# Kernel tuning notes

Hardware: AMD Instinct MI355X
Metric: run time of the kernel (lower is better)

The kernel has to match this reference:

```python
import jax, jax.numpy as jnp
import numpy as np

L, N, S, C = 128, 8, 16384, 256   # queries, batch, pixels (128x128), d_model
B, V = 256, 256                   # bottleneck channels, value depth
EPS_NORM = 1e-12                  # F.normalize eps
EPS_LN = 1e-5                     # LayerNorm eps


def _xavier(key, fan_out, fan_in):
    lim = np.sqrt(6.0 / (fan_in + fan_out)).astype(np.float32)
    return jax.random.uniform(key, (fan_out, fan_in), jnp.float32, -lim, lim)


def setup_inputs() -> dict:
    key = jax.random.key(0)
    ks = jax.random.split(key, 8)
    return {
        "tgt": jax.random.normal(ks[0], (L, N, C), jnp.float32),
        "memory": jax.random.normal(ks[1], (S, N, C), jnp.float32),
        "pos": jax.random.normal(ks[2], (S, N, C), jnp.float32),
        "query_pos": jax.random.normal(ks[3], (L, N, C), jnp.float32),
        "Wq": _xavier(ks[4], B, C), "bq": jnp.zeros((B,), jnp.float32),
        "Wp": _xavier(ks[5], B, C), "bp": jnp.zeros((B,), jnp.float32),
        "Wv": _xavier(ks[6], V, B), "bv": jnp.zeros((V,), jnp.float32),
        "Wo": _xavier(ks[7], C, V), "bo": jnp.zeros((C,), jnp.float32),
        "gamma": jnp.ones((C,), jnp.float32),
        "beta": jnp.zeros((C,), jnp.float32),
    }


def reference(tgt, memory, pos, query_pos, Wq, bq, Wp, bp, Wv, bv, Wo, bo, gamma, beta):
    q = tgt + query_pos                       # (L,N,C)
    k = memory + pos                          # (S,N,C)
    q_proj = q @ Wq.T + bq                    # (L,N,B)
    k_proj = k @ Wp.T + bp                    # (S,N,B)
    v_proj = k_proj @ Wv.T + bv               # (S,N,V)
    # F.normalize(k_proj, p=2, dim=-1)
    k_norm = k_proj / jnp.maximum(
        jnp.linalg.norm(k_proj, axis=-1, keepdims=True), EPS_NORM)
    mask_logits = jnp.einsum('lnc,snc->nls', q_proj, k_norm)  # (N,L,S)
    # hard top-1 assignment (detached in torch); one-hot einsum == direct gather
    idx = jnp.argmax(mask_logits, axis=-1)    # (N,L) int
    v_t = jnp.transpose(v_proj, (1, 0, 2))    # (N,S,V)
    kmeans = jnp.take_along_axis(v_t, idx[:, :, None], axis=1)  # (N,L,V)
    kmeans = jnp.transpose(kmeans, (1, 0, 2))  # (L,N,V)
    upd = kmeans @ Wo.T + bo                  # (L,N,C)
    x = tgt + upd                             # dropout p=0 -> identity
    mu = jnp.mean(x, axis=-1, keepdims=True)
    var = jnp.var(x, axis=-1, keepdims=True)
    return (x - mu) / jnp.sqrt(var + EPS_LN) * gamma + beta
```

## Files before the change

kernel.cpp:

```cpp
#include <hip/hip_runtime.h>
#include <stdint.h>

#define L_Q 128
#define N_B 8
#define S_P 16384

typedef _Float16 half8 __attribute__((ext_vector_type(8)));
typedef float f32x4 __attribute__((ext_vector_type(4)));


__global__ __launch_bounds__(256) void k_prep(
    const float* __restrict__ Wp, const float* __restrict__ Wv,
    const float* __restrict__ Wo,
    float* __restrict__ WpT, float* __restrict__ WvT, float* __restrict__ WoT,
    _Float16* __restrict__ Wp_hi, _Float16* __restrict__ Wp_lo,
    unsigned long long* __restrict__ packed) {
  int idx = (blockIdx.x << 8) + threadIdx.x;
  int r = idx >> 8, c = idx & 255;
  int t = (c << 8) + r;
  float wp = Wp[idx];
  WpT[t] = wp;
  WvT[t] = Wv[idx];
  WoT[t] = Wo[idx];
  _Float16 h = (_Float16)wp;
  Wp_hi[idx] = h;
  Wp_lo[idx] = (_Float16)(wp - (float)h);
  if (idx < N_B * L_Q) packed[idx] = 0ull;
}

__global__ __launch_bounds__(256) void k_qproj(
    const float* __restrict__ tgt, const float* __restrict__ qpos,
    const float* __restrict__ Wq, const float* __restrict__ bq,
    _Float16* __restrict__ q_hi, _Float16* __restrict__ q_lo) {
  __shared__ __align__(16) float q_lds[4][256];
  int tid = threadIdx.x;
  int r0 = blockIdx.x << 2;
  #pragma unroll
  for (int j = 0; j < 4; ++j) {
    int p = (j << 8) + tid;
    int rl = p >> 8, c = p & 255;
    int g = ((r0 + rl) << 8) + c;
    q_lds[rl][c] = tgt[g] + qpos[g];
  }
  __syncthreads();
  float bqv = bq[tid];
  float a0 = bqv, a1 = bqv, a2 = bqv, a3 = bqv;
  #pragma unroll 4
  for (int c = 0; c < 256; c += 4) {
    float4 w = *(const float4*)(Wq + (tid << 8) + c);
    a0 = fmaf(w.x, q_lds[0][c], fmaf(w.y, q_lds[0][c+1],
         fmaf(w.z, q_lds[0][c+2], fmaf(w.w, q_lds[0][c+3], a0))));
    a1 = fmaf(w.x, q_lds[1][c], fmaf(w.y, q_lds[1][c+1],
         fmaf(w.z, q_lds[1][c+2], fmaf(w.w, q_lds[1][c+3], a1))));
    a2 = fmaf(w.x, q_lds[2][c], fmaf(w.y, q_lds[2][c+1],
         fmaf(w.z, q_lds[2][c+2], fmaf(w.w, q_lds[2][c+3], a2))));
    a3 = fmaf(w.x, q_lds[3][c], fmaf(w.y, q_lds[3][c+1],
         fmaf(w.z, q_lds[3][c+2], fmaf(w.w, q_lds[3][c+3], a3))));
  }
  float av[4] = {a0, a1, a2, a3};
  #pragma unroll
  for (int rl = 0; rl < 4; ++rl) {
    int r = r0 + rl;
    int l = r >> 3, nn = r & 7;
    int o = (((nn << 7) + l) << 8) + tid;
    _Float16 h = (_Float16)av[rl];
    q_hi[o] = h;
    q_lo[o] = (_Float16)(av[rl] - (float)h);
  }
}

__global__ __launch_bounds__(256, 2) void k_main(
    const float* __restrict__ memory, const float* __restrict__ pos,
    const _Float16* __restrict__ Wp_hi, const _Float16* __restrict__ Wp_lo,
    const float* __restrict__ bp,
    const _Float16* __restrict__ q_hi, const _Float16* __restrict__ q_lo,
    unsigned long long* __restrict__ packed) {
  __shared__ __align__(16) unsigned short smu[2 * 64 * 256];
  unsigned short* a_hi = smu;
  unsigned short* a_lo = smu + 16384;

  int tid = threadIdx.x;
  int w = tid >> 6;
  int lane = tid & 63;
  int l15 = lane & 15, quad = lane >> 4;
  int n = blockIdx.y;
  int s_base = blockIdx.x << 6;

  {
    int half = tid >> 5;
    int chunk = tid & 31;
    int c0 = chunk << 3;
    #pragma unroll
    for (int it = 0; it < 8; ++it) {
      int srow = (it << 3) + half;
      int g = (((s_base + srow) << 3) + n) * 256 + c0;
      float4 m0 = *(const float4*)(memory + g);
      float4 m1 = *(const float4*)(memory + g + 4);
      float4 p0 = *(const float4*)(pos + g);
      float4 p1 = *(const float4*)(pos + g + 4);
      float f[8] = {m0.x + p0.x, m0.y + p0.y, m0.z + p0.z, m0.w + p0.w,
                    m1.x + p1.x, m1.y + p1.y, m1.z + p1.z, m1.w + p1.w};
      half8 hv, lv;
      #pragma unroll
      for (int j = 0; j < 8; ++j) {
        _Float16 h = (_Float16)f[j];
        hv[j] = h;
        lv[j] = (_Float16)(f[j] - (float)h);
      }
      int p = chunk ^ (srow & 15);
      *(half8*)(a_hi + (srow << 8) + (p << 3)) = hv;
      *(half8*)(a_lo + (srow << 8) + (p << 3)) = lv;
    }
  }
  __syncthreads();

  f32x4 acc1[4][4];
  #pragma unroll
  for (int m = 0; m < 4; ++m)
    #pragma unroll
    for (int bn = 0; bn < 4; ++bn) acc1[m][bn] = (f32x4)(0.0f);

  for (int kk = 0; kk < 8; ++kk) {
    int cofs = (kk << 5) + (quad << 3);
    half8 ah[4], al[4];
    #pragma unroll
    for (int m = 0; m < 4; ++m) {
      int s = (m << 4) + l15;
      int p = (cofs >> 3) ^ l15;
      ah[m] = *(const half8*)(a_hi + (s << 8) + (p << 3));
      al[m] = *(const half8*)(a_lo + (s << 8) + (p << 3));
    }
    #pragma unroll
    for (int bn = 0; bn < 4; ++bn) {
      int b = (w << 6) + (bn << 4) + l15;
      half8 wh = *(const half8*)(Wp_hi + (b << 8) + cofs);
      half8 wl = *(const half8*)(Wp_lo + (b << 8) + cofs);
      #pragma unroll
      for (int m = 0; m < 4; ++m) {
        acc1[m][bn] = __builtin_amdgcn_mfma_f32_16x16x32_f16(ah[m], wh, acc1[m][bn], 0, 0, 0);
        acc1[m][bn] = __builtin_amdgcn_mfma_f32_16x16x32_f16(ah[m], wl, acc1[m][bn], 0, 0, 0);
        acc1[m][bn] = __builtin_amdgcn_mfma_f32_16x16x32_f16(al[m], wh, acc1[m][bn], 0, 0, 0);
      }
    }
  }

  float bpv[4];
  #pragma unroll
  for (int bn = 0; bn < 4; ++bn) bpv[bn] = bp[(w << 6) + (bn << 4) + l15];
  float n2[4][4];
  #pragma unroll
  for (int m = 0; m < 4; ++m)
    #pragma unroll
    for (int r = 0; r < 4; ++r) {
      float s = 0.f;
      #pragma unroll
      for (int bn = 0; bn < 4; ++bn) {
        float v = acc1[m][bn][r] + bpv[bn];
        acc1[m][bn][r] = v;
        s = fmaf(v, v, s);
      }
      n2[m][r] = s;
    }
  #pragma unroll
  for (int off = 1; off < 16; off <<= 1)
    #pragma unroll
    for (int m = 0; m < 4; ++m)
      #pragma unroll
      for (int r = 0; r < 4; ++r) n2[m][r] += __shfl_xor(n2[m][r], off, 64);

  __syncthreads();
  if (l15 == 0) {
    #pragma unroll
    for (int m = 0; m < 4; ++m)
      #pragma unroll
      for (int r = 0; r < 4; ++r) {
        int i = (w << 6) + (m << 4) + (quad << 2) + r;
        unsigned u = __float_as_uint(n2[m][r]);
        smu[i << 1] = (unsigned short)u;
        smu[(i << 1) + 1] = (unsigned short)(u >> 16);
      }
  }
  __syncthreads();
  float rn[4][4];
  #pragma unroll
  for (int m = 0; m < 4; ++m)
    #pragma unroll
    for (int r = 0; r < 4; ++r) {
      int s = (m << 4) + (quad << 2) + r;
      float t = 0.f;
      #pragma unroll
      for (int ww = 0; ww < 4; ++ww) {
        int i = (ww << 6) + s;
        unsigned u = (unsigned)smu[i << 1] | ((unsigned)smu[(i << 1) + 1] << 16);
        t += __uint_as_float(u);
      }
      rn[m][r] = 1.f / fmaxf(sqrtf(t), 1e-12f);
    }
  __syncthreads();

  unsigned short* kn_hi = smu;
  unsigned short* kn_lo = smu + 16384;
  #pragma unroll
  for (int m = 0; m < 4; ++m)
    #pragma unroll
    for (int bn = 0; bn < 4; ++bn)
      #pragma unroll
      for (int r = 0; r < 4; ++r) {
        int s = (m << 4) + (quad << 2) + r;
        int b = (w << 6) + (bn << 4) + l15;
        float v = acc1[m][bn][r] * rn[m][r];
        _Float16 h = (_Float16)v;
        _Float16 lo = (_Float16)(v - (float)h);
        int p = (b >> 3) ^ (s & 15);
        int off = (s << 8) + (p << 3) + (b & 7);
        *(_Float16*)(kn_hi + off) = h;
        *(_Float16*)(kn_lo + off) = lo;
      }
  __syncthreads();

  f32x4 acc2[2][4];
  #pragma unroll
  for (int m = 0; m < 2; ++m)
    #pragma unroll
    for (int sn = 0; sn < 4; ++sn) acc2[m][sn] = (f32x4)(0.0f);

  const _Float16* qhb = q_hi + (n << 15);
  const _Float16* qlb = q_lo + (n << 15);
  for (int kk = 0; kk < 8; ++kk) {
    int b0 = (kk << 5) + (quad << 3);
    half8 qh[2], ql[2];
    #pragma unroll
    for (int m = 0; m < 2; ++m) {
      int l = (w << 5) + (m << 4) + l15;
      qh[m] = *(const half8*)(qhb + (l << 8) + b0);
      ql[m] = *(const half8*)(qlb + (l << 8) + b0);
    }
    #pragma unroll
    for (int sn = 0; sn < 4; ++sn) {
      int s = (sn << 4) + l15;
      int p = (b0 >> 3) ^ l15;
      half8 kh = *(const half8*)(kn_hi + (s << 8) + (p << 3));
      half8 kl = *(const half8*)(kn_lo + (s << 8) + (p << 3));
      #pragma unroll
      for (int m = 0; m < 2; ++m) {
        acc2[m][sn] = __builtin_amdgcn_mfma_f32_16x16x32_f16(qh[m], kh, acc2[m][sn], 0, 0, 0);
        acc2[m][sn] = __builtin_amdgcn_mfma_f32_16x16x32_f16(qh[m], kl, acc2[m][sn], 0, 0, 0);
        acc2[m][sn] = __builtin_amdgcn_mfma_f32_16x16x32_f16(ql[m], kh, acc2[m][sn], 0, 0, 0);
      }
    }
  }

  float mv[8];
  int mi[8];
  #pragma unroll
  for (int m = 0; m < 2; ++m)
    #pragma unroll
    for (int r = 0; r < 4; ++r) {
      int i = (m << 2) + r;
      mv[i] = acc2[m][0][r];
      mi[i] = s_base + l15;
      #pragma unroll
      for (int sn = 1; sn < 4; ++sn) {
        float v = acc2[m][sn][r];
        int si = s_base + (sn << 4) + l15;
        if (v > mv[i]) { mv[i] = v; mi[i] = si; }
      }
    }
  #pragma unroll
  for (int off = 1; off < 16; off <<= 1)
    #pragma unroll
    for (int i = 0; i < 8; ++i) {
      float ov = __shfl_xor(mv[i], off, 64);
      int oi = __shfl_xor(mi[i], off, 64);
      if (ov > mv[i] || (ov == mv[i] && oi < mi[i])) { mv[i] = ov; mi[i] = oi; }
    }
  if (l15 == 0) {
    #pragma unroll
    for (int i = 0; i < 8; ++i) {
      int m = i >> 2, r = i & 3;
      int l = (w << 5) + (m << 4) + (quad << 2) + r;
      unsigned ub = __float_as_uint(mv[i]);
      ub = (ub & 0x80000000u) ? ~ub : (ub | 0x80000000u);
      unsigned long long pk = ((unsigned long long)ub << 32) |
                              (unsigned long long)(16383u - (unsigned)mi[i]);
      atomicMax(packed + (n << 7) + l, pk);
    }
  }
}

__global__ __launch_bounds__(256) void k_final(
    const float* __restrict__ tgt,
    const float* __restrict__ memory, const float* __restrict__ pos,
    const float* __restrict__ WpT, const float* __restrict__ bp,
    const float* __restrict__ WvT, const float* __restrict__ bv,
    const float* __restrict__ WoT, const float* __restrict__ bo,
    const float* __restrict__ gamma, const float* __restrict__ beta,
    const unsigned long long* __restrict__ packed, float* __restrict__ out) {
  __shared__ __align__(16) float buf0[4][256];
  __shared__ __align__(16) float buf1[4][256];
  __shared__ __align__(16) float buf2[4][256];
  __shared__ float red[4][4][2];
  int tid = threadIdx.x;
  int r0 = blockIdx.x << 2;

  #pragma unroll
  for (int j = 0; j < 4; ++j) {
    int p = (j << 8) + tid;
    int rl = p >> 8, c = p & 255;
    int r = r0 + rl;
    int l = r >> 3, nn = r & 7;
    unsigned long long pk = packed[(nn << 7) + l];
    int sstar = (16383 - (int)(unsigned int)(pk & 0xffffffffu)) & 16383;
    int g = ((sstar << 3) + nn) * 256 + c;
    buf0[rl][c] = memory[g] + pos[g];
  }
  __syncthreads();

  float a[4];
  { float b0v = bp[tid];
    #pragma unroll
    for (int rl = 0; rl < 4; ++rl) a[rl] = b0v; }
  #pragma unroll 4
  for (int c = 0; c < 256; ++c) {
    float w = WpT[(c << 8) + tid];
    #pragma unroll
    for (int rl = 0; rl < 4; ++rl) a[rl] = fmaf(w, buf0[rl][c], a[rl]);
  }
  #pragma unroll
  for (int rl = 0; rl < 4; ++rl) buf1[rl][tid] = a[rl];
  __syncthreads();

  { float b0v = bv[tid];
    #pragma unroll
    for (int rl = 0; rl < 4; ++rl) a[rl] = b0v; }
  #pragma unroll 4
  for (int c = 0; c < 256; ++c) {
    float w = WvT[(c << 8) + tid];
    #pragma unroll
    for (int rl = 0; rl < 4; ++rl) a[rl] = fmaf(w, buf1[rl][c], a[rl]);
  }
  #pragma unroll
  for (int rl = 0; rl < 4; ++rl) buf2[rl][tid] = a[rl];
  __syncthreads();

  { float b0v = bo[tid];
    #pragma unroll
    for (int rl = 0; rl < 4; ++rl) a[rl] = b0v; }
  #pragma unroll 4
  for (int c = 0; c < 256; ++c) {
    float w = WoT[(c << 8) + tid];
    #pragma unroll
    for (int rl = 0; rl < 4; ++rl) a[rl] = fmaf(w, buf2[rl][c], a[rl]);
  }
  float x[4];
  #pragma unroll
  for (int rl = 0; rl < 4; ++rl)
    x[rl] = tgt[((r0 + rl) << 8) + tid] + a[rl];

  float s1[4], s2[4];
  #pragma unroll
  for (int rl = 0; rl < 4; ++rl) { s1[rl] = x[rl]; s2[rl] = x[rl] * x[rl]; }
  #pragma unroll
  for (int off = 1; off < 64; off <<= 1)
    #pragma unroll
    for (int rl = 0; rl < 4; ++rl) {
      s1[rl] += __shfl_xor(s1[rl], off, 64);
      s2[rl] += __shfl_xor(s2[rl], off, 64);
    }
  int wv = tid >> 6, ln = tid & 63;
  if (ln == 0) {
    #pragma unroll
    for (int rl = 0; rl < 4; ++rl) { red[wv][rl][0] = s1[rl]; red[wv][rl][1] = s2[rl]; }
  }
  __syncthreads();
  float g = gamma[tid], be = beta[tid];
  #pragma unroll
  for (int rl = 0; rl < 4; ++rl) {
    float S1 = red[0][rl][0] + red[1][rl][0] + red[2][rl][0] + red[3][rl][0];
    float S2 = red[0][rl][1] + red[1][rl][1] + red[2][rl][1] + red[3][rl][1];
    float mu = S1 * (1.f / 256.f);
    float var = S2 * (1.f / 256.f) - mu * mu;
    float rs = rsqrtf(var + 1e-5f);
    out[((r0 + rl) << 8) + tid] = (x[rl] - mu) * rs * g + be;
  }
}

extern "C" void kernel_launch(void* const* d_in, const int* in_sizes, int n_in,
                              void* d_out, int out_size, void* d_ws, size_t ws_size,
                              hipStream_t stream) {
  const float* tgt    = (const float*)d_in[0];
  const float* memory = (const float*)d_in[1];
  const float* pos    = (const float*)d_in[2];
  const float* qpos   = (const float*)d_in[3];
  const float* Wq     = (const float*)d_in[4];
  const float* bq     = (const float*)d_in[5];
  const float* Wp     = (const float*)d_in[6];
  const float* bp     = (const float*)d_in[7];
  const float* Wv     = (const float*)d_in[8];
  const float* bv     = (const float*)d_in[9];
  const float* Wo     = (const float*)d_in[10];
  const float* bo     = (const float*)d_in[11];
  const float* gamma  = (const float*)d_in[12];
  const float* beta   = (const float*)d_in[13];

  float* ws = (float*)d_ws;
  float* WpT = ws;
  float* WvT = ws + 65536;
  float* WoT = ws + 131072;
  _Float16* Wp_hi = (_Float16*)(ws + 196608);
  _Float16* Wp_lo = (_Float16*)(ws + 229376);
  _Float16* q_hi  = (_Float16*)(ws + 262144);
  _Float16* q_lo  = (_Float16*)(ws + 393216);
  unsigned long long* packed = (unsigned long long*)(ws + 524288);
  float* out = (float*)d_out;

  k_prep<<<256, 256, 0, stream>>>(Wp, Wv, Wo, WpT, WvT, WoT, Wp_hi, Wp_lo, packed);
  k_qproj<<<256, 256, 0, stream>>>(tgt, qpos, Wq, bq, q_hi, q_lo);
  dim3 gb(S_P / 64, N_B);
  k_main<<<gb, 256, 0, stream>>>(memory, pos, Wp_hi, Wp_lo, bp, q_hi, q_lo, packed);
  k_final<<<256, 256, 0, stream>>>(tgt, memory, pos, WpT, bp, WvT, bv,
                                   WoT, bo, gamma, beta, packed, out);
}
```

Measured before the change: 503.2 us.

## Halve k_main pixel tile for occupancy, merge prep and qproj kernels

Each k_main block now handles 32 pixels instead of 64. This halves LDS use and accumulator registers and raises the occupancy hint to 4 blocks per CU. The norm reduction uses a dedicated small shared array, which removes two block barriers. The weight-prep and query-projection kernels are fused into one launch to save a launch. In exchange, each block reloads the Wp and q fragments for half as many pixels, doubling global/L2 traffic for those operands, and there are twice as many atomic argmax updates.

```diff
diff --git a/kernel.cpp b/kernel.cpp
--- a/kernel.cpp
+++ b/kernel.cpp
@@ -9,32 +9,32 @@
 typedef float f32x4 __attribute__((ext_vector_type(4)));
 
 
-__global__ __launch_bounds__(256) void k_prep(
+__global__ __launch_bounds__(256) void k_prep_qproj(
     const float* __restrict__ Wp, const float* __restrict__ Wv,
     const float* __restrict__ Wo,
     float* __restrict__ WpT, float* __restrict__ WvT, float* __restrict__ WoT,
     _Float16* __restrict__ Wp_hi, _Float16* __restrict__ Wp_lo,
-    unsigned long long* __restrict__ packed) {
-  int idx = (blockIdx.x << 8) + threadIdx.x;
-  int r = idx >> 8, c = idx & 255;
-  int t = (c << 8) + r;
-  float wp = Wp[idx];
-  WpT[t] = wp;
-  WvT[t] = Wv[idx];
-  WoT[t] = Wo[idx];
-  _Float16 h = (_Float16)wp;
-  Wp_hi[idx] = h;
-  Wp_lo[idx] = (_Float16)(wp - (float)h);
-  if (idx < N_B * L_Q) packed[idx] = 0ull;
-}
-
-__global__ __launch_bounds__(256) void k_qproj(
+    unsigned long long* __restrict__ packed,
     const float* __restrict__ tgt, const float* __restrict__ qpos,
     const float* __restrict__ Wq, const float* __restrict__ bq,
     _Float16* __restrict__ q_hi, _Float16* __restrict__ q_lo) {
   __shared__ __align__(16) float q_lds[4][256];
   int tid = threadIdx.x;
-  int r0 = blockIdx.x << 2;
+  if (blockIdx.x < 256) {
+    int idx = (blockIdx.x << 8) + tid;
+    int r = idx >> 8, c = idx & 255;
+    int t = (c << 8) + r;
+    float wp = Wp[idx];
+    WpT[t] = wp;
+    WvT[t] = Wv[idx];
+    WoT[t] = Wo[idx];
+    _Float16 h = (_Float16)wp;
+    Wp_hi[idx] = h;
+    Wp_lo[idx] = (_Float16)(wp - (float)h);
+    if (idx < N_B * L_Q) packed[idx] = 0ull;
+    return;
+  }
+  int r0 = (blockIdx.x - 256) << 2;
   #pragma unroll
   for (int j = 0; j < 4; ++j) {
     int p = (j << 8) + tid;
@@ -69,29 +69,30 @@
   }
 }
 
-__global__ __launch_bounds__(256, 2) void k_main(
+__global__ __launch_bounds__(256, 4) void k_main(
     const float* __restrict__ memory, const float* __restrict__ pos,
     const _Float16* __restrict__ Wp_hi, const _Float16* __restrict__ Wp_lo,
     const float* __restrict__ bp,
     const _Float16* __restrict__ q_hi, const _Float16* __restrict__ q_lo,
     unsigned long long* __restrict__ packed) {
-  __shared__ __align__(16) unsigned short smu[2 * 64 * 256];
+  __shared__ __align__(16) unsigned short smu[2 * 32 * 256];
+  __shared__ float snorm[4][32];
   unsigned short* a_hi = smu;
-  unsigned short* a_lo = smu + 16384;
+  unsigned short* a_lo = smu + 8192;
 
   int tid = threadIdx.x;
   int w = tid >> 6;
   int lane = tid & 63;
   int l15 = lane & 15, quad = lane >> 4;
   int n = blockIdx.y;
-  int s_base = blockIdx.x << 6;
+  int s_base = blockIdx.x << 5;
 
   {
     int half = tid >> 5;
     int chunk = tid & 31;
     int c0 = chunk << 3;
     #pragma unroll
-    for (int it = 0; it < 8; ++it) {
+    for (int it = 0; it < 4; ++it) {
       int srow = (it << 3) + half;
       int g = (((s_base + srow) << 3) + n) * 256 + c0;
       float4 m0 = *(const float4*)(memory + g);
@@ -114,17 +115,17 @@
   }
   __syncthreads();
 
-  f32x4 acc1[4][4];
-  #pragma unroll
-  for (int m = 0; m < 4; ++m)
+  f32x4 acc1[2][4];
+  #pragma unroll
+  for (int m = 0; m < 2; ++m)
     #pragma unroll
     for (int bn = 0; bn < 4; ++bn) acc1[m][bn] = (f32x4)(0.0f);
 
   for (int kk = 0; kk < 8; ++kk) {
     int cofs = (kk << 5) + (quad << 3);
-    half8 ah[4], al[4];
-    #pragma unroll
-    for (int m = 0; m < 4; ++m) {
+    half8 ah[2], al[2];
+    #pragma unroll
+    for (int m = 0; m < 2; ++m) {
       int s = (m << 4) + l15;
       int p = (cofs >> 3) ^ l15;
       ah[m] = *(const half8*)(a_hi + (s << 8) + (p << 3));
@@ -136,7 +137,7 @@
       half8 wh = *(const half8*)(Wp_hi + (b << 8) + cofs);
       half8 wl = *(const half8*)(Wp_lo + (b << 8) + cofs);
       #pragma unroll
-      for (int m = 0; m < 4; ++m) {
+      for (int m = 0; m < 2; ++m) {
         acc1[m][bn] = __builtin_amdgcn_mfma_f32_16x16x32_f16(ah[m], wh, acc1[m][bn], 0, 0, 0);
         acc1[m][bn] = __builtin_amdgcn_mfma_f32_16x16x32_f16(ah[m], wl, acc1[m][bn], 0, 0, 0);
         acc1[m][bn] = __builtin_amdgcn_mfma_f32_16x16x32_f16(al[m], wh, acc1[m][bn], 0, 0, 0);
@@ -147,9 +148,9 @@
   float bpv[4];
   #pragma unroll
   for (int bn = 0; bn < 4; ++bn) bpv[bn] = bp[(w << 6) + (bn << 4) + l15];
-  float n2[4][4];
-  #pragma unroll
-  for (int m = 0; m < 4; ++m)
+  float n2[2][4];
+  #pragma unroll
+  for (int m = 0; m < 2; ++m)
     #pragma unroll
     for (int r = 0; r < 4; ++r) {
       float s = 0.f;
@@ -164,44 +165,32 @@
   #pragma unroll
   for (int off = 1; off < 16; off <<= 1)
     #pragma unroll
-    for (int m = 0; m < 4; ++m)
+    for (int m = 0; m < 2; ++m)
       #pragma unroll
       for (int r = 0; r < 4; ++r) n2[m][r] += __shfl_xor(n2[m][r], off, 64);
 
-  __syncthreads();
   if (l15 == 0) {
     #pragma unroll
-    for (int m = 0; m < 4; ++m)
-      #pragma unroll
-      for (int r = 0; r < 4; ++r) {
-        int i = (w << 6) + (m << 4) + (quad << 2) + r;
-        unsigned u = __float_as_uint(n2[m][r]);
-        smu[i << 1] = (unsigned short)u;
-        smu[(i << 1) + 1] = (unsigned short)(u >> 16);
-      }
-  }
-  __syncthreads();
-  float rn[4][4];
-  #pragma unroll
-  for (int m = 0; m < 4; ++m)
+    for (int m = 0; m < 2; ++m)
+      #pragma unroll
+      for (int r = 0; r < 4; ++r)
+        snorm[w][(m << 4) + (quad << 2) + r] = n2[m][r];
+  }
+  __syncthreads();
+  float rn[2][4];
+  #pragma unroll
+  for (int m = 0; m < 2; ++m)
     #pragma unroll
     for (int r = 0; r < 4; ++r) {
       int s = (m << 4) + (quad << 2) + r;
-      float t = 0.f;
-      #pragma unroll
-      for (int ww = 0; ww < 4; ++ww) {
-        int i = (ww << 6) + s;
-        unsigned u = (unsigned)smu[i << 1] | ((unsigned)smu[(i << 1) + 1] << 16);
-        t += __uint_as_float(u);
-      }
+      float t = snorm[0][s] + snorm[1][s] + snorm[2][s] + snorm[3][s];
       rn[m][r] = 1.f / fmaxf(sqrtf(t), 1e-12f);
     }
-  __syncthreads();
 
   unsigned short* kn_hi = smu;
-  unsigned short* kn_lo = smu + 16384;
-  #pragma unroll
-  for (int m = 0; m < 4; ++m)
+  unsigned short* kn_lo = smu + 8192;
+  #pragma unroll
+  for (int m = 0; m < 2; ++m)
     #pragma unroll
     for (int bn = 0; bn < 4; ++bn)
       #pragma unroll
@@ -218,11 +207,11 @@
       }
   __syncthreads();
 
-  f32x4 acc2[2][4];
-  #pragma unroll
-  for (int m = 0; m < 2; ++m)
-    #pragma unroll
-    for (int sn = 0; sn < 4; ++sn) acc2[m][sn] = (f32x4)(0.0f);
+  f32x4 acc2[2][2];
+  #pragma unroll
+  for (int m = 0; m < 2; ++m)
+    #pragma unroll
+    for (int sn = 0; sn < 2; ++sn) acc2[m][sn] = (f32x4)(0.0f);
 
   const _Float16* qhb = q_hi + (n << 15);
   const _Float16* qlb = q_lo + (n << 15);
@@ -236,7 +225,7 @@
       ql[m] = *(const half8*)(qlb + (l << 8) + b0);
     }
     #pragma unroll
-    for (int sn = 0; sn < 4; ++sn) {
+    for (int sn = 0; sn < 2; ++sn) {
       int s = (sn << 4) + l15;
       int p = (b0 >> 3) ^ l15;
       half8 kh = *(const half8*)(kn_hi + (s << 8) + (p << 3));
@@ -259,12 +248,9 @@
       int i = (m << 2) + r;
       mv[i] = acc2[m][0][r];
       mi[i] = s_base + l15;
-      #pragma unroll
-      for (int sn = 1; sn < 4; ++sn) {
-        float v = acc2[m][sn][r];
-        int si = s_base + (sn << 4) + l15;
-        if (v > mv[i]) { mv[i] = v; mi[i] = si; }
-      }
+      float v = acc2[m][1][r];
+      int si = s_base + 16 + l15;
+      if (v > mv[i]) { mv[i] = v; mi[i] = si; }
     }
   #pragma unroll
   for (int off = 1; off < 16; off <<= 1)
@@ -414,9 +400,10 @@
   unsigned long long* packed = (unsigned long long*)(ws + 524288);
   float* out = (float*)d_out;
 
-  k_prep<<<256, 256, 0, stream>>>(Wp, Wv, Wo, WpT, WvT, WoT, Wp_hi, Wp_lo, packed);
-  k_qproj<<<256, 256, 0, stream>>>(tgt, qpos, Wq, bq, q_hi, q_lo);
-  dim3 gb(S_P / 64, N_B);
+  k_prep_qproj<<<512, 256, 0, stream>>>(Wp, Wv, Wo, WpT, WvT, WoT,
+                                        Wp_hi, Wp_lo, packed,
+                                        tgt, qpos, Wq, bq, q_hi, q_lo);
+  dim3 gb(S_P / 32, N_B);
   k_main<<<gb, 256, 0, stream>>>(memory, pos, Wp_hi, Wp_lo, bp, q_hi, q_lo, packed);
   k_final<<<256, 256, 0, stream>>>(tgt, memory, pos, WpT, bp, WvT, bv,
                                    WoT, bo, gamma, beta, packed, out);
```

Measured after the change: 567.8 us. 12.8% more time.
